# Kernel tuning notes

Hardware: AMD Instinct MI355X
Metric: run time of the kernel (lower is better)

## Reference

```python
import jax, jax.numpy as jnp
import numpy as np

D_MODEL = 1024
N_HEADS = 16
HEAD_DIM = D_MODEL // N_HEADS


def setup_inputs() -> dict:
    key = jax.random.key(0)
    k_x, k_qkv, k_out = jax.random.split(key, 3)
    x = jax.random.normal(k_x, (4, 2048, D_MODEL), dtype=jnp.float32)
    # nn.Linear weights are (out_features, in_features); init std=0.02
    w_qkv = jax.random.normal(k_qkv, (3 * D_MODEL, D_MODEL), dtype=jnp.float32) * 0.02
    w_out = jax.random.normal(k_out, (D_MODEL, D_MODEL), dtype=jnp.float32) * 0.02
    return {"x": x, "w_qkv": w_qkv, "w_out": w_out}


def reference(x, w_qkv, w_out):
    B, T, C = x.shape
    H, Dh = N_HEADS, HEAD_DIM
    # qkv projection: x @ w_qkv.T -> (B, T, 3C)
    qkv = jnp.einsum('btc,oc->bto', x, w_qkv)
    q, k, v = jnp.split(qkv, 3, axis=-1)

    def split_heads(t):
        return t.reshape(B, T, H, Dh).transpose(0, 2, 1, 3)  # (B, H, T, Dh)

    q, k, v = split_heads(q), split_heads(k), split_heads(v)
    scale = jnp.sqrt(jnp.asarray(Dh, dtype=x.dtype))
    scores = jnp.einsum('bhqd,bhkd->bhqk', q, k) / scale  # (B, H, T, T)
    causal = jnp.tril(jnp.ones((T, T), dtype=bool))
    scores = jnp.where(causal[None, None], scores, jnp.asarray(-jnp.inf, dtype=scores.dtype))
    attn = jax.nn.softmax(scores, axis=-1)
    out = jnp.einsum('bhqk,bhkd->bhqd', attn, v)  # (B, H, T, Dh)
    out = out.transpose(0, 2, 1, 3).reshape(B, T, C)
    return jnp.einsum('btc,oc->bto', out, w_out)
```

## Files before the change

### kernel.cpp

```cpp
#include <hip/hip_runtime.h>

typedef __attribute__((ext_vector_type(8))) short bf16x8;
typedef __attribute__((ext_vector_type(4))) float f32x4;
typedef __attribute__((ext_vector_type(16))) float f32x16;
typedef __attribute__((ext_vector_type(4))) int i32x4;
using u16 = unsigned short;

constexpr int Bsz = 4, T = 2048, C = 1024, H = 16, Dh = 64;
constexpr int Mrows = Bsz * T;
constexpr int K_DIM = 1024;
constexpr float QSCALE = 0.18033688011112042f;

__device__ inline u16 f2bf(float f) {
    unsigned u = __builtin_bit_cast(unsigned, f);
    u += 0x7FFFu + ((u >> 16) & 1u);
    return (u16)(u >> 16);
}

__device__ inline void g2l16(const void* g, void* l) {
    __builtin_amdgcn_global_load_lds((const __attribute__((address_space(1))) void*)g,
                                     (__attribute__((address_space(3))) void*)l, 16, 0, 0);
}

__device__ inline unsigned pk2(float lo, float hi) {
    unsigned d;
    asm("v_cvt_pk_bf16_f32 %0, %1, %2" : "=v"(d) : "v"(lo), "v"(hi));
    return d;
}
__device__ inline void swap32(unsigned& a, unsigned& b) {
    asm("v_permlane32_swap_b32 %0, %1" : "+v"(a), "+v"(b));
}

__global__ __launch_bounds__(256)
void cvt_k(const float* __restrict__ x, const float* __restrict__ wq,
           const float* __restrict__ wo, u16* __restrict__ xb,
           u16* __restrict__ wqb, u16* __restrict__ wob)
{
    int idx = blockIdx.x * 256 + threadIdx.x;
    const float* src; u16* dst; int rel;
    if (idx < 1048576)      { src = x;  dst = xb;  rel = idx; }
    else if (idx < 1441792) { src = wq; dst = wqb; rel = idx - 1048576; }
    else                    { src = wo; dst = wob; rel = idx - 1441792; }
    size_t off = (size_t)rel * 8;
    float4 a = *(const float4*)(src + off);
    float4 b = *(const float4*)(src + off + 4);
    unsigned r0 = (unsigned)f2bf(a.x) | ((unsigned)f2bf(a.y) << 16);
    unsigned r1 = (unsigned)f2bf(a.z) | ((unsigned)f2bf(a.w) << 16);
    unsigned r2 = (unsigned)f2bf(b.x) | ((unsigned)f2bf(b.y) << 16);
    unsigned r3 = (unsigned)f2bf(b.z) | ((unsigned)f2bf(b.w) << 16);
    *(uint4*)(dst + off) = make_uint4(r0, r1, r2, r3);
}

__device__ __forceinline__ bf16x8 rdfrag(const u16* base, int row, int kc, int lhi) {
    int byte = row * 128 + kc * 64 + lhi * 16;
    byte ^= (row & 7) << 4;
    return *(const bf16x8*)((const char*)base + byte);
}

__device__ __forceinline__ void stg_half(u16* ldsbase, const u16* gb, int tid) {
    #pragma unroll
    for (int it2 = 0; it2 < 2; ++it2) {
        int i = it2 * 512 + tid;
        int r = i >> 3, c8 = i & 7;
        int sc = c8 ^ (r & 7);
        g2l16(gb + (size_t)r * K_DIM + sc * 8,
              ldsbase + (size_t)(it2 * 512 + (tid & 448)) * 8);
    }
}

__device__ __forceinline__ void rdAf(bf16x8 (&af)[4][2], const u16* base,
                                     int r0, int lane16, int lhi) {
    #pragma unroll
    for (int mi = 0; mi < 4; ++mi)
        #pragma unroll
        for (int kc = 0; kc < 2; ++kc)
            af[mi][kc] = rdfrag(base, r0 + mi * 16 + lane16, kc, lhi);
}

__device__ __forceinline__ void rdBf(bf16x8 (&bf2)[2][2], const u16* base,
                                     int r0, int lane16, int lhi) {
    #pragma unroll
    for (int ni = 0; ni < 2; ++ni)
        #pragma unroll
        for (int kc = 0; kc < 2; ++kc)
            bf2[ni][kc] = rdfrag(base, r0 + ni * 16 + lane16, kc, lhi);
}

__device__ __forceinline__ void mfma_quad(f32x4 (&acc)[8][4], const bf16x8 (&af)[4][2],
                                          const bf16x8 (&bf2)[2][2], int rh, int ch) {
    #pragma unroll
    for (int kc = 0; kc < 2; ++kc)
        #pragma unroll
        for (int mi = 0; mi < 4; ++mi)
            #pragma unroll
            for (int ni = 0; ni < 2; ++ni)
                acc[rh * 4 + mi][ch * 2 + ni] = __builtin_amdgcn_mfma_f32_16x16x32_bf16(
                    af[mi][kc], bf2[ni][kc], acc[rh * 4 + mi][ch * 2 + ni], 0, 0, 0);
}

__device__ __forceinline__ void ph_open() {
    __builtin_amdgcn_s_barrier();
    asm volatile("s_waitcnt lgkmcnt(0)" ::: "memory");
    __builtin_amdgcn_sched_barrier(0);
}
__device__ __forceinline__ void ph_close() {
    __builtin_amdgcn_s_barrier();
    __builtin_amdgcn_sched_barrier(0);
}

__global__ __launch_bounds__(512, 2)
void gemm_qk8(const u16* __restrict__ xb, const u16* __restrict__ wqkvb,
              u16* __restrict__ qws, u16* __restrict__ kws)
{
    __shared__ alignas(16) u16 As[2][256 * 64];
    __shared__ alignas(16) u16 Bs2[2][256 * 64];

    const int tid = threadIdx.x;
    const int l = tid & 63, wid = tid >> 6;
    const int wm = wid >> 2, wn = wid & 3;
    const int lane16 = l & 15, lhi = l >> 4;
    const int m0 = blockIdx.x * 256, n0 = blockIdx.y * 256;

    const u16* Ab = xb + (size_t)m0 * K_DIM;
    const u16* Bb = wqkvb + (size_t)n0 * K_DIM;

    f32x4 acc[8][4] = {};
    bf16x8 af[4][2];
    bf16x8 bfr[2][2][2];

    stg_half(&As[0][0],     Ab, tid);
    stg_half(&As[0][8192],  Ab + (size_t)128 * K_DIM, tid);
    stg_half(&Bs2[0][0],    Bb, tid);
    stg_half(&Bs2[0][8192], Bb + (size_t)128 * K_DIM, tid);
    stg_half(&Bs2[1][0],    Bb + 64, tid);
    asm volatile("s_waitcnt vmcnt(2)" ::: "memory");
    __builtin_amdgcn_s_barrier();
    __builtin_amdgcn_sched_barrier(0);

    for (int it = 0; it < 8; ++it) {
        const int ka = it * 128;
        const bool more = (it < 7);

        rdAf(af, As[0], wm * 128, lane16, lhi);
        rdBf(bfr[0], Bs2[0], wn * 64, lane16, lhi);
        stg_half(&Bs2[1][8192], Bb + (size_t)128 * K_DIM + ka + 64, tid);
        ph_open();
        __builtin_amdgcn_s_setprio(1);
        mfma_quad(acc, af, bfr[0], 0, 0);
        __builtin_amdgcn_s_setprio(0);
        ph_close();

        rdBf(bfr[1], Bs2[0], wn * 64 + 32, lane16, lhi);
        stg_half(&As[1][0], Ab + ka + 64, tid);
        ph_open();
        __builtin_amdgcn_s_setprio(1);
        mfma_quad(acc, af, bfr[1], 0, 1);
        __builtin_amdgcn_s_setprio(0);
        ph_close();

        rdAf(af, As[0], wm * 128 + 64, lane16, lhi);
        stg_half(&As[1][8192], Ab + (size_t)128 * K_DIM + ka + 64, tid);
        ph_open();
        __builtin_amdgcn_s_setprio(1);
        mfma_quad(acc, af, bfr[1], 1, 1);
        __builtin_amdgcn_s_setprio(0);
        ph_close();

        if (more) stg_half(&Bs2[0][0], Bb + ka + 128, tid);
        ph_open();
        __builtin_amdgcn_s_setprio(1);
        mfma_quad(acc, af, bfr[0], 1, 0);
        __builtin_amdgcn_s_setprio(0);
        if (more) asm volatile("s_waitcnt vmcnt(2)" ::: "memory");
        else      asm volatile("s_waitcnt vmcnt(0)" ::: "memory");
        ph_close();

        rdAf(af, As[1], wm * 128, lane16, lhi);
        rdBf(bfr[0], Bs2[1], wn * 64, lane16, lhi);
        if (more) stg_half(&Bs2[0][8192], Bb + (size_t)128 * K_DIM + ka + 128, tid);
        ph_open();
        __builtin_amdgcn_s_setprio(1);
        mfma_quad(acc, af, bfr[0], 0, 0);
        __builtin_amdgcn_s_setprio(0);
        ph_close();

        rdBf(bfr[1], Bs2[1], wn * 64 + 32, lane16, lhi);
        if (more) stg_half(&As[0][0], Ab + ka + 128, tid);
        ph_open();
        __builtin_amdgcn_s_setprio(1);
        mfma_quad(acc, af, bfr[1], 0, 1);
        __builtin_amdgcn_s_setprio(0);
        ph_close();

        rdAf(af, As[1], wm * 128 + 64, lane16, lhi);
        if (more) stg_half(&As[0][8192], Ab + (size_t)128 * K_DIM + ka + 128, tid);
        ph_open();
        __builtin_amdgcn_s_setprio(1);
        mfma_quad(acc, af, bfr[1], 1, 1);
        __builtin_amdgcn_s_setprio(0);
        ph_close();

        if (more) stg_half(&Bs2[1][0], Bb + ka + 192, tid);
        ph_open();
        __builtin_amdgcn_s_setprio(1);
        mfma_quad(acc, af, bfr[0], 1, 0);
        __builtin_amdgcn_s_setprio(0);
        if (more) asm volatile("s_waitcnt vmcnt(2)" ::: "memory");
        else      asm volatile("s_waitcnt vmcnt(0)" ::: "memory");
        ph_close();
    }

    #pragma unroll
    for (int a = 0; a < 8; ++a)
        #pragma unroll
        for (int bc = 0; bc < 4; ++bc)
            #pragma unroll
            for (int r = 0; r < 4; ++r) {
                int gm = m0 + wm * 128 + a * 16 + lhi * 4 + r;
                int gn = n0 + wn * 64 + bc * 16 + lane16;
                float val = acc[a][bc][r];
                int hh = (gn >> 6) & 15, d = gn & 63;
                int bb = gm >> 11, t = gm & 2047;
                size_t off = (((size_t)bb * H + hh) * T + t) * Dh + d;
                if (gn < C) qws[off] = f2bf(val * QSCALE);
                else        kws[off] = f2bf(val);
            }
}

__device__ inline void stage_g(u16* lds, const u16* gb, int ldg, int tid) {
    #pragma unroll
    for (int i = 0; i < 4; ++i) {
        int ch = i * 256 + tid;
        int r = ch >> 3, c8 = ch & 7;
        int sc = c8 ^ (r & 7);
        g2l16(gb + (size_t)r * ldg + sc * 8, lds + (i * 256 + (tid & 192)) * 8);
    }
}

template<int MODE>
__device__ __forceinline__
void gemm_body(const u16* __restrict__ Ab, const u16* __restrict__ Bb,
               float* __restrict__ Op, u16* __restrict__ vtws,
               u16* As, u16* Bs, int m0, int n0)
{
    const int tid = threadIdx.x;
    const int l = tid & 63, wid = tid >> 6;
    const int wm = wid >> 1, wn = wid & 1;
    const int lane16 = l & 15, lhi = l >> 4;

    const u16* Abase = Ab + (size_t)m0 * K_DIM;
    const u16* Bbase = Bb + (size_t)n0 * K_DIM;

    f32x4 acc[4][4] = {};

    for (int ks = 0; ks < K_DIM / 64; ++ks) {
        __syncthreads();
        stage_g(As, Abase + ks * 64, K_DIM, tid);
        stage_g(Bs, Bbase + ks * 64, K_DIM, tid);
        __syncthreads();
        #pragma unroll
        for (int kc = 0; kc < 2; kc++) {
            bf16x8 af[4], bfr[4];
            #pragma unroll
            for (int mi = 0; mi < 4; mi++) {
                int row = wm * 64 + mi * 16 + lane16;
                int byte = row * 128 + kc * 64 + lhi * 16; byte ^= (row & 7) << 4;
                af[mi] = *(const bf16x8*)((const char*)As + byte);
            }
            #pragma unroll
            for (int ni = 0; ni < 4; ni++) {
                int row = wn * 64 + ni * 16 + lane16;
                int byte = row * 128 + kc * 64 + lhi * 16; byte ^= (row & 7) << 4;
                bfr[ni] = *(const bf16x8*)((const char*)Bs + byte);
            }
            #pragma unroll
            for (int mi = 0; mi < 4; mi++)
                #pragma unroll
                for (int ni = 0; ni < 4; ni++) {
                    if constexpr (MODE == 2)
                        acc[mi][ni] = __builtin_amdgcn_mfma_f32_16x16x32_bf16(
                            bfr[ni], af[mi], acc[mi][ni], 0, 0, 0);
                    else
                        acc[mi][ni] = __builtin_amdgcn_mfma_f32_16x16x32_bf16(
                            af[mi], bfr[ni], acc[mi][ni], 0, 0, 0);
                }
        }
    }

    if constexpr (MODE == 2) {
        #pragma unroll
        for (int mi = 0; mi < 4; mi++)
            #pragma unroll
            for (int ni = 0; ni < 4; ni++)
                #pragma unroll
                for (int r = 0; r < 4; r++) {
                    int wr = n0 + wn * 64 + ni * 16 + lhi * 4 + r;
                    int tg = m0 + wm * 64 + mi * 16 + lane16;
                    int hh = (wr >> 6) & 15, d = wr & 63;
                    int bb = tg >> 11, tt = tg & 2047;
                    size_t off = (((size_t)bb * H + hh) * Dh + d) * T + tt;
                    vtws[off] = f2bf(acc[mi][ni][r]);
                }
    } else {
        #pragma unroll
        for (int mi = 0; mi < 4; mi++)
            #pragma unroll
            for (int ni = 0; ni < 4; ni++)
                #pragma unroll
                for (int r = 0; r < 4; r++) {
                    int gm = m0 + wm * 64 + mi * 16 + lhi * 4 + r;
                    int gn = n0 + wn * 64 + ni * 16 + lane16;
                    Op[(size_t)gm * C + gn] = acc[mi][ni][r];
                }
    }
}

__global__ __launch_bounds__(256)
void gemm_v(const u16* __restrict__ xb, const u16* __restrict__ wqkvb,
            u16* __restrict__ vtws)
{
    __shared__ alignas(16) u16 As[128 * 64];
    __shared__ alignas(16) u16 Bs[128 * 64];
    gemm_body<2>(xb, wqkvb, nullptr, vtws, As, Bs,
                 blockIdx.x * 128, 2 * C + blockIdx.y * 128);
}

__global__ __launch_bounds__(256)
void gemm_out(const u16* __restrict__ ob, const u16* __restrict__ woutb,
              float* __restrict__ Op)
{
    __shared__ alignas(16) u16 As[128 * 64];
    __shared__ alignas(16) u16 Bs[128 * 64];
    gemm_body<1>(ob, woutb, Op, nullptr, As, Bs,
                 blockIdx.x * 128, blockIdx.y * 128);
}

constexpr float SMAX = 16.0f;

__device__ inline void stage_c(u16* lds, const u16* gb, int rstride, int tid) {
    #pragma unroll
    for (int it = 0; it < 2; ++it) {
        int i = it * 256 + tid;
        int r = i & 63, c8 = i >> 6;
        g2l16(gb + (size_t)r * rstride + c8 * 8, lds + i * 8);
    }
}

__global__ __launch_bounds__(256, 3)
void attn_k(const u16* __restrict__ qws, const u16* __restrict__ kws,
            const u16* __restrict__ vtws, u16* __restrict__ ows)
{
    __shared__ alignas(16) u16 KL[3][64 * 64];
    __shared__ alignas(16) u16 VL[3][64 * 64];

    const int bid = blockIdx.x;
    const int head = bid & 63;
    const int qt = 15 - (bid >> 6);
    const int b = head >> 4, h = head & 15;
    const int tid = threadIdx.x, w = tid >> 6, l = tid & 63;
    const int l31 = l & 31, hi = l >> 5;

    const size_t hoff = (size_t)head * (T * Dh);
    const u16* Qg  = qws + hoff;
    const u16* Kg  = kws + hoff;
    const u16* Vtg = vtws + hoff;

    const int qb = qt * 128;
    const int nt = 2 * qt + 2;
    const int qbw = qb + w * 32;

    bf16x8 qf[4];
    #pragma unroll
    for (int c = 0; c < 4; ++c)
        qf[c] = *(const bf16x8*)(Qg + (size_t)(qbw + l31) * Dh + c * 16 + hi * 8);

    f32x16 o0{}, o1{};
    float lrun = 0.f;

    stage_c(KL[0], Kg, Dh, tid);
    stage_c(VL[0], Vtg, T, tid);
    stage_c(KL[1], Kg + (size_t)64 * Dh, Dh, tid);
    stage_c(VL[1], Vtg + 64, T, tid);

    int cur = 0;
    for (int t = 0; t < nt; ++t) {
        if (t + 1 < nt) asm volatile("s_waitcnt vmcnt(4)" ::: "memory");
        else            asm volatile("s_waitcnt vmcnt(0)" ::: "memory");
        __builtin_amdgcn_s_barrier();
        __builtin_amdgcn_sched_barrier(0);

        int nx = cur + 2; if (nx >= 3) nx -= 3;
        if (t + 2 < nt) {
            stage_c(KL[nx], Kg + (size_t)(t + 2) * 64 * Dh, Dh, tid);
            stage_c(VL[nx], Vtg + (t + 2) * 64, T, tid);
        }

        const int kv0 = t * 64;
        if (kv0 <= qbw + 31) {
            const char* Kb = (const char*)KL[cur];
            const char* Vb = (const char*)VL[cur];

            bf16x8 kf0[4], kf1[4];
            #pragma unroll
            for (int c = 0; c < 4; ++c) {
                int off = (c * 2 + hi) * 1024 + l31 * 16;
                kf0[c] = *(const bf16x8*)(Kb + off);
                kf1[c] = *(const bf16x8*)(Kb + off + 512);
            }

            f32x16 s0{}, s1{};
            __builtin_amdgcn_s_setprio(1);
            #pragma unroll
            for (int c = 0; c < 4; ++c) {
                s0 = __builtin_amdgcn_mfma_f32_32x32x16_bf16(kf0[c], qf[c], s0, 0, 0, 0);
                s1 = __builtin_amdgcn_mfma_f32_32x32x16_bf16(kf1[c], qf[c], s1, 0, 0, 0);
            }
            __builtin_amdgcn_s_setprio(0);

            if (kv0 + 63 > qbw) {
                int qg = qbw + l31;
                #pragma unroll
                for (int r = 0; r < 16; ++r) {
                    int kvg = kv0 + (r & 3) + 8 * (r >> 2) + 4 * hi;
                    if (kvg > qg)      s0[r] = -__builtin_inff();
                    if (kvg + 32 > qg) s1[r] = -__builtin_inff();
                }
            }

            float p0[16], p1[16];
            float t0 = 0.f, t1 = 0.f, t2 = 0.f, t3 = 0.f;
            #pragma unroll
            for (int r = 0; r < 16; ++r) {
                p0[r] = __builtin_amdgcn_exp2f(s0[r] - SMAX);
                p1[r] = __builtin_amdgcn_exp2f(s1[r] - SMAX);
                float s = p0[r] + p1[r];
                if ((r & 3) == 0) t0 += s; else if ((r & 3) == 1) t1 += s;
                else if ((r & 3) == 2) t2 += s; else t3 += s;
            }
            lrun += (t0 + t1) + (t2 + t3);

            unsigned paf[4][4];
            unsigned cc[8];
            #pragma unroll
            for (int i = 0; i < 4; ++i) cc[i]     = pk2(p0[2 * i], p0[2 * i + 1]);
            #pragma unroll
            for (int i = 0; i < 4; ++i) cc[4 + i] = pk2(p0[8 + 2 * i], p0[9 + 2 * i]);
            swap32(cc[0], cc[2]); swap32(cc[1], cc[3]);
            swap32(cc[4], cc[6]); swap32(cc[5], cc[7]);
            #pragma unroll
            for (int i = 0; i < 4; ++i) { paf[0][i] = cc[i]; paf[1][i] = cc[4 + i]; }
            #pragma unroll
            for (int i = 0; i < 4; ++i) cc[i]     = pk2(p1[2 * i], p1[2 * i + 1]);
            #pragma unroll
            for (int i = 0; i < 4; ++i) cc[4 + i] = pk2(p1[8 + 2 * i], p1[9 + 2 * i]);
            swap32(cc[0], cc[2]); swap32(cc[1], cc[3]);
            swap32(cc[4], cc[6]); swap32(cc[5], cc[7]);
            #pragma unroll
            for (int i = 0; i < 4; ++i) { paf[2][i] = cc[i]; paf[3][i] = cc[4 + i]; }

            __builtin_amdgcn_s_setprio(1);
            #pragma unroll
            for (int kb = 0; kb < 4; ++kb) {
                i32x4 wv = {(int)paf[kb][0], (int)paf[kb][1],
                            (int)paf[kb][2], (int)paf[kb][3]};
                bf16x8 pa = __builtin_bit_cast(bf16x8, wv);
                int off = (kb * 2 + hi) * 1024 + l31 * 16;
                bf16x8 v0 = *(const bf16x8*)(Vb + off);
                bf16x8 v1 = *(const bf16x8*)(Vb + off + 512);
                o0 = __builtin_amdgcn_mfma_f32_32x32x16_bf16(pa, v0, o0, 0, 0, 0);
                o1 = __builtin_amdgcn_mfma_f32_32x32x16_bf16(pa, v1, o1, 0, 0, 0);
            }
            __builtin_amdgcn_s_setprio(0);
        }
        cur = (cur == 2) ? 0 : cur + 1;
    }

    float lt = lrun + __shfl_xor(lrun, 32);
    float inv = 1.0f / lt;
    #pragma unroll
    for (int r = 0; r < 16; ++r) {
        int cr = (r & 3) + 8 * (r >> 2) + 4 * hi;
        float il = __shfl(inv, cr);
        size_t rowoff = ((size_t)b * T + qb + w * 32 + cr) * C + h * Dh + l31;
        ows[rowoff]      = f2bf(o0[r] * il);
        ows[rowoff + 32] = f2bf(o1[r] * il);
    }
}

extern "C" void kernel_launch(void* const* d_in, const int* in_sizes, int n_in,
                              void* d_out, int out_size, void* d_ws, size_t ws_size,
                              hipStream_t stream)
{
    const float* x     = (const float*)d_in[0];
    const float* w_qkv = (const float*)d_in[1];
    const float* w_out = (const float*)d_in[2];
    float* out = (float*)d_out;

    const size_t SZ = (size_t)Bsz * H * T * Dh;
    u16* qws   = (u16*)d_ws;
    u16* kws   = qws + SZ;
    u16* vtws  = kws + SZ;
    u16* xb    = vtws + SZ;
    u16* ows   = xb;
    u16* wqkvb = xb + SZ;
    u16* woutb = wqkvb + (size_t)3 * C * C;

    cvt_k<<<dim3(6144), 256, 0, stream>>>(x, w_qkv, w_out, xb, wqkvb, woutb);

    gemm_qk8<<<dim3(Mrows / 256, (2 * C) / 256), 512, 0, stream>>>(xb, wqkvb, qws, kws);
    gemm_v<<<dim3(Mrows / 128, C / 128), 256, 0, stream>>>(xb, wqkvb, vtws);

    attn_k<<<dim3(1024), 256, 0, stream>>>(qws, kws, vtws, ows);

    gemm_out<<<dim3(Mrows / 128, C / 128), 256, 0, stream>>>(ows, woutb, out);
}
```

Before: 154.9 us.

## Software-pipeline attention loop: QK^T of tile t overlapped with softmax/PV of t-1

Restructures the causal attention inner loop so each iteration issues the QK^T MFMAs for the current KV tile while the exp, packing and PV MFMAs run for the previous tile's saved scores. V tiles are now staged one tile ahead instead of two, and a final drain step finishes the last tile after the loop. The goal is to hide softmax VALU/transcendental latency behind matrix-core work. It costs extra live registers for the carried score accumulators and drops the setprio hints.

```diff
diff --git a/kernel.cpp b/kernel.cpp
--- a/kernel.cpp
+++ b/kernel.cpp
@@ -376,30 +376,73 @@
 
     f32x16 o0{}, o1{};
     float lrun = 0.f;
+    f32x16 sp0{}, sp1{};
+
+    auto fin = [&](int slot) {
+        const char* Vb = (const char*)VL[slot];
+        float p0[16], p1[16];
+        float t0 = 0.f, t1 = 0.f, t2 = 0.f, t3 = 0.f;
+        #pragma unroll
+        for (int r = 0; r < 16; ++r) {
+            p0[r] = __builtin_amdgcn_exp2f(sp0[r] - SMAX);
+            p1[r] = __builtin_amdgcn_exp2f(sp1[r] - SMAX);
+            float s = p0[r] + p1[r];
+            if ((r & 3) == 0) t0 += s; else if ((r & 3) == 1) t1 += s;
+            else if ((r & 3) == 2) t2 += s; else t3 += s;
+        }
+        lrun += (t0 + t1) + (t2 + t3);
+
+        unsigned paf[4][4];
+        unsigned cc[8];
+        #pragma unroll
+        for (int i = 0; i < 4; ++i) cc[i]     = pk2(p0[2 * i], p0[2 * i + 1]);
+        #pragma unroll
+        for (int i = 0; i < 4; ++i) cc[4 + i] = pk2(p0[8 + 2 * i], p0[9 + 2 * i]);
+        swap32(cc[0], cc[2]); swap32(cc[1], cc[3]);
+        swap32(cc[4], cc[6]); swap32(cc[5], cc[7]);
+        #pragma unroll
+        for (int i = 0; i < 4; ++i) { paf[0][i] = cc[i]; paf[1][i] = cc[4 + i]; }
+        #pragma unroll
+        for (int i = 0; i < 4; ++i) cc[i]     = pk2(p1[2 * i], p1[2 * i + 1]);
+        #pragma unroll
+        for (int i = 0; i < 4; ++i) cc[4 + i] = pk2(p1[8 + 2 * i], p1[9 + 2 * i]);
+        swap32(cc[0], cc[2]); swap32(cc[1], cc[3]);
+        swap32(cc[4], cc[6]); swap32(cc[5], cc[7]);
+        #pragma unroll
+        for (int i = 0; i < 4; ++i) { paf[2][i] = cc[i]; paf[3][i] = cc[4 + i]; }
+
+        #pragma unroll
+        for (int kb = 0; kb < 4; ++kb) {
+            i32x4 wv = {(int)paf[kb][0], (int)paf[kb][1],
+                        (int)paf[kb][2], (int)paf[kb][3]};
+            bf16x8 pa = __builtin_bit_cast(bf16x8, wv);
+            int off = (kb * 2 + hi) * 1024 + l31 * 16;
+            bf16x8 v0 = *(const bf16x8*)(Vb + off);
+            bf16x8 v1 = *(const bf16x8*)(Vb + off + 512);
+            o0 = __builtin_amdgcn_mfma_f32_32x32x16_bf16(pa, v0, o0, 0, 0, 0);
+            o1 = __builtin_amdgcn_mfma_f32_32x32x16_bf16(pa, v1, o1, 0, 0, 0);
+        }
+    };
 
     stage_c(KL[0], Kg, Dh, tid);
+    stage_c(KL[1], Kg + (size_t)64 * Dh, Dh, tid);
     stage_c(VL[0], Vtg, T, tid);
-    stage_c(KL[1], Kg + (size_t)64 * Dh, Dh, tid);
-    stage_c(VL[1], Vtg + 64, T, tid);
-
-    int cur = 0;
+
     for (int t = 0; t < nt; ++t) {
         if (t + 1 < nt) asm volatile("s_waitcnt vmcnt(4)" ::: "memory");
         else            asm volatile("s_waitcnt vmcnt(0)" ::: "memory");
         __builtin_amdgcn_s_barrier();
         __builtin_amdgcn_sched_barrier(0);
 
-        int nx = cur + 2; if (nx >= 3) nx -= 3;
-        if (t + 2 < nt) {
-            stage_c(KL[nx], Kg + (size_t)(t + 2) * 64 * Dh, Dh, tid);
-            stage_c(VL[nx], Vtg + (t + 2) * 64, T, tid);
-        }
+        int tp2 = t + 2; while (tp2 >= 3) tp2 -= 3;
+        int tp1 = t + 1; while (tp1 >= 3) tp1 -= 3;
+        int tm1 = t + 2; while (tm1 >= 3) tm1 -= 3;
+        if (t + 2 < nt) stage_c(KL[tp2], Kg + (size_t)(t + 2) * 64 * Dh, Dh, tid);
+        if (t + 1 < nt) stage_c(VL[tp1], Vtg + (t + 1) * 64, T, tid);
 
         const int kv0 = t * 64;
         if (kv0 <= qbw + 31) {
-            const char* Kb = (const char*)KL[cur];
-            const char* Vb = (const char*)VL[cur];
-
+            const char* Kb = (const char*)KL[t % 3];
             bf16x8 kf0[4], kf1[4];
             #pragma unroll
             for (int c = 0; c < 4; ++c) {
@@ -427,52 +470,15 @@
                 }
             }
 
-            float p0[16], p1[16];
-            float t0 = 0.f, t1 = 0.f, t2 = 0.f, t3 = 0.f;
-            #pragma unroll
-            for (int r = 0; r < 16; ++r) {
-                p0[r] = __builtin_amdgcn_exp2f(s0[r] - SMAX);
-                p1[r] = __builtin_amdgcn_exp2f(s1[r] - SMAX);
-                float s = p0[r] + p1[r];
-                if ((r & 3) == 0) t0 += s; else if ((r & 3) == 1) t1 += s;
-                else if ((r & 3) == 2) t2 += s; else t3 += s;
-            }
-            lrun += (t0 + t1) + (t2 + t3);
-
-            unsigned paf[4][4];
-            unsigned cc[8];
-            #pragma unroll
-            for (int i = 0; i < 4; ++i) cc[i]     = pk2(p0[2 * i], p0[2 * i + 1]);
-            #pragma unroll
-            for (int i = 0; i < 4; ++i) cc[4 + i] = pk2(p0[8 + 2 * i], p0[9 + 2 * i]);
-            swap32(cc[0], cc[2]); swap32(cc[1], cc[3]);
-            swap32(cc[4], cc[6]); swap32(cc[5], cc[7]);
-            #pragma unroll
-            for (int i = 0; i < 4; ++i) { paf[0][i] = cc[i]; paf[1][i] = cc[4 + i]; }
-            #pragma unroll
-            for (int i = 0; i < 4; ++i) cc[i]     = pk2(p1[2 * i], p1[2 * i + 1]);
-            #pragma unroll
-            for (int i = 0; i < 4; ++i) cc[4 + i] = pk2(p1[8 + 2 * i], p1[9 + 2 * i]);
-            swap32(cc[0], cc[2]); swap32(cc[1], cc[3]);
-            swap32(cc[4], cc[6]); swap32(cc[5], cc[7]);
-            #pragma unroll
-            for (int i = 0; i < 4; ++i) { paf[2][i] = cc[i]; paf[3][i] = cc[4 + i]; }
-
-            __builtin_amdgcn_s_setprio(1);
-            #pragma unroll
-            for (int kb = 0; kb < 4; ++kb) {
-                i32x4 wv = {(int)paf[kb][0], (int)paf[kb][1],
-                            (int)paf[kb][2], (int)paf[kb][3]};
-                bf16x8 pa = __builtin_bit_cast(bf16x8, wv);
-                int off = (kb * 2 + hi) * 1024 + l31 * 16;
-                bf16x8 v0 = *(const bf16x8*)(Vb + off);
-                bf16x8 v1 = *(const bf16x8*)(Vb + off + 512);
-                o0 = __builtin_amdgcn_mfma_f32_32x32x16_bf16(pa, v0, o0, 0, 0, 0);
-                o1 = __builtin_amdgcn_mfma_f32_32x32x16_bf16(pa, v1, o1, 0, 0, 0);
-            }
-            __builtin_amdgcn_s_setprio(0);
+            if (t > 0) fin(tm1);
+            sp0 = s0; sp1 = s1;
+        } else if (kv0 <= qbw + 95) {
+            fin(tm1);
         }
-        cur = (cur == 2) ? 0 : cur + 1;
+    }
+    if ((nt - 1) * 64 <= qbw + 31) {
+        int slot = nt - 1; while (slot >= 3) slot -= 3;
+        fin(slot);
     }
 
     float lt = lrun + __shfl_xor(lrun, 32);
```

New measurement: 155.3 us. About the same (+0.2%).

## Double attention query tile per block to reuse staged K/V across two query subtiles

Applied to the files above, without the earlier changes.

Each attention block now handles 256 query rows (64 per wave, two 32-row subtiles) instead of 128. The grid halves to 512 blocks. Every K/V tile staged into LDS and every K/V fragment loaded into registers now feeds two query subtiles, which halves global-to-LDS K/V traffic and LDS fragment reads per unit of work. In exchange, register pressure rises (launch bounds drop from 3 to 2 blocks per CU), the grid is smaller, and causal load imbalance across blocks grows.

```diff
diff --git a/kernel.cpp b/kernel.cpp
--- a/kernel.cpp
+++ b/kernel.cpp
@@ -346,7 +346,7 @@
     }
 }
 
-__global__ __launch_bounds__(256, 3)
+__global__ __launch_bounds__(256, 2)
 void attn_k(const u16* __restrict__ qws, const u16* __restrict__ kws,
             const u16* __restrict__ vtws, u16* __restrict__ ows)
 {
@@ -355,7 +355,7 @@
 
     const int bid = blockIdx.x;
     const int head = bid & 63;
-    const int qt = 15 - (bid >> 6);
+    const int qt = 7 - (bid >> 6);
     const int b = head >> 4, h = head & 15;
     const int tid = threadIdx.x, w = tid >> 6, l = tid & 63;
     const int l31 = l & 31, hi = l >> 5;
@@ -365,17 +365,20 @@
     const u16* Kg  = kws + hoff;
     const u16* Vtg = vtws + hoff;
 
-    const int qb = qt * 128;
-    const int nt = 2 * qt + 2;
-    const int qbw = qb + w * 32;
-
-    bf16x8 qf[4];
-    #pragma unroll
-    for (int c = 0; c < 4; ++c)
-        qf[c] = *(const bf16x8*)(Qg + (size_t)(qbw + l31) * Dh + c * 16 + hi * 8);
-
-    f32x16 o0{}, o1{};
-    float lrun = 0.f;
+    const int qb = qt * 256;
+    const int nt = 4 * qt + 4;
+    const int qbw = qb + w * 64;
+
+    bf16x8 qf[2][4];
+    #pragma unroll
+    for (int q2 = 0; q2 < 2; ++q2)
+        #pragma unroll
+        for (int c = 0; c < 4; ++c)
+            qf[q2][c] = *(const bf16x8*)(Qg + (size_t)(qbw + q2 * 32 + l31) * Dh
+                                         + c * 16 + hi * 8);
+
+    f32x16 oq[2][2] = {};
+    float lrun[2] = {0.f, 0.f};
 
     stage_c(KL[0], Kg, Dh, tid);
     stage_c(VL[0], Vtg, T, tid);
@@ -396,94 +399,102 @@
         }
 
         const int kv0 = t * 64;
-        if (kv0 <= qbw + 31) {
+        if (kv0 <= qbw + 63) {
             const char* Kb = (const char*)KL[cur];
             const char* Vb = (const char*)VL[cur];
 
-            bf16x8 kf0[4], kf1[4];
+            bf16x8 kf0[4], kf1[4], vf0[4], vf1[4];
             #pragma unroll
             for (int c = 0; c < 4; ++c) {
                 int off = (c * 2 + hi) * 1024 + l31 * 16;
                 kf0[c] = *(const bf16x8*)(Kb + off);
                 kf1[c] = *(const bf16x8*)(Kb + off + 512);
+                vf0[c] = *(const bf16x8*)(Vb + off);
+                vf1[c] = *(const bf16x8*)(Vb + off + 512);
             }
 
-            f32x16 s0{}, s1{};
-            __builtin_amdgcn_s_setprio(1);
-            #pragma unroll
-            for (int c = 0; c < 4; ++c) {
-                s0 = __builtin_amdgcn_mfma_f32_32x32x16_bf16(kf0[c], qf[c], s0, 0, 0, 0);
-                s1 = __builtin_amdgcn_mfma_f32_32x32x16_bf16(kf1[c], qf[c], s1, 0, 0, 0);
+            #pragma unroll
+            for (int q2 = 0; q2 < 2; ++q2) {
+                const int qbb = qbw + q2 * 32;
+                if (kv0 > qbb + 31) continue;
+
+                f32x16 s0{}, s1{};
+                __builtin_amdgcn_s_setprio(1);
+                #pragma unroll
+                for (int c = 0; c < 4; ++c) {
+                    s0 = __builtin_amdgcn_mfma_f32_32x32x16_bf16(kf0[c], qf[q2][c], s0, 0, 0, 0);
+                    s1 = __builtin_amdgcn_mfma_f32_32x32x16_bf16(kf1[c], qf[q2][c], s1, 0, 0, 0);
+                }
+                __builtin_amdgcn_s_setprio(0);
+
+                if (kv0 + 63 > qbb) {
+                    int qg = qbb + l31;
+                    #pragma unroll
+                    for (int r = 0; r < 16; ++r) {
+                        int kvg = kv0 + (r & 3) + 8 * (r >> 2) + 4 * hi;
+                        if (kvg > qg)      s0[r] = -__builtin_inff();
+                        if (kvg + 32 > qg) s1[r] = -__builtin_inff();
+                    }
+                }
+
+                float p0[16], p1[16];
+                float t0 = 0.f, t1 = 0.f, t2 = 0.f, t3 = 0.f;
+                #pragma unroll
+                for (int r = 0; r < 16; ++r) {
+                    p0[r] = __builtin_amdgcn_exp2f(s0[r] - SMAX);
+                    p1[r] = __builtin_amdgcn_exp2f(s1[r] - SMAX);
+                    float s = p0[r] + p1[r];
+                    if ((r & 3) == 0) t0 += s; else if ((r & 3) == 1) t1 += s;
+                    else if ((r & 3) == 2) t2 += s; else t3 += s;
+                }
+                lrun[q2] += (t0 + t1) + (t2 + t3);
+
+                unsigned paf[4][4];
+                unsigned cc[8];
+                #pragma unroll
+                for (int i = 0; i < 4; ++i) cc[i]     = pk2(p0[2 * i], p0[2 * i + 1]);
+                #pragma unroll
+                for (int i = 0; i < 4; ++i) cc[4 + i] = pk2(p0[8 + 2 * i], p0[9 + 2 * i]);
+                swap32(cc[0], cc[2]); swap32(cc[1], cc[3]);
+                swap32(cc[4], cc[6]); swap32(cc[5], cc[7]);
+                #pragma unroll
+                for (int i = 0; i < 4; ++i) { paf[0][i] = cc[i]; paf[1][i] = cc[4 + i]; }
+                #pragma unroll
+                for (int i = 0; i < 4; ++i) cc[i]     = pk2(p1[2 * i], p1[2 * i + 1]);
+                #pragma unroll
+                for (int i = 0; i < 4; ++i) cc[4 + i] = pk2(p1[8 + 2 * i], p1[9 + 2 * i]);
+                swap32(cc[0], cc[2]); swap32(cc[1], cc[3]);
+                swap32(cc[4], cc[6]); swap32(cc[5], cc[7]);
+                #pragma unroll
+                for (int i = 0; i < 4; ++i) { paf[2][i] = cc[i]; paf[3][i] = cc[4 + i]; }
+
+                __builtin_amdgcn_s_setprio(1);
+                #pragma unroll
+                for (int kb = 0; kb < 4; ++kb) {
+                    i32x4 wv = {(int)paf[kb][0], (int)paf[kb][1],
+                                (int)paf[kb][2], (int)paf[kb][3]};
+                    bf16x8 pa = __builtin_bit_cast(bf16x8, wv);
+                    oq[q2][0] = __builtin_amdgcn_mfma_f32_32x32x16_bf16(pa, vf0[kb], oq[q2][0], 0, 0, 0);
+                    oq[q2][1] = __builtin_amdgcn_mfma_f32_32x32x16_bf16(pa, vf1[kb], oq[q2][1], 0, 0, 0);
+                }
+                __builtin_amdgcn_s_setprio(0);
             }
-            __builtin_amdgcn_s_setprio(0);
-
-            if (kv0 + 63 > qbw) {
-                int qg = qbw + l31;
-                #pragma unroll
-                for (int r = 0; r < 16; ++r) {
-                    int kvg = kv0 + (r & 3) + 8 * (r >> 2) + 4 * hi;
-                    if (kvg > qg)      s0[r] = -__builtin_inff();
-                    if (kvg + 32 > qg) s1[r] = -__builtin_inff();
-                }
-            }
-
-            float p0[16], p1[16];
-            float t0 = 0.f, t1 = 0.f, t2 = 0.f, t3 = 0.f;
-            #pragma unroll
-            for (int r = 0; r < 16; ++r) {
-                p0[r] = __builtin_amdgcn_exp2f(s0[r] - SMAX);
-                p1[r] = __builtin_amdgcn_exp2f(s1[r] - SMAX);
-                float s = p0[r] + p1[r];
-                if ((r & 3) == 0) t0 += s; else if ((r & 3) == 1) t1 += s;
-                else if ((r & 3) == 2) t2 += s; else t3 += s;
-            }
-            lrun += (t0 + t1) + (t2 + t3);
-
-            unsigned paf[4][4];
-            unsigned cc[8];
-            #pragma unroll
-            for (int i = 0; i < 4; ++i) cc[i]     = pk2(p0[2 * i], p0[2 * i + 1]);
-            #pragma unroll
-            for (int i = 0; i < 4; ++i) cc[4 + i] = pk2(p0[8 + 2 * i], p0[9 + 2 * i]);
-            swap32(cc[0], cc[2]); swap32(cc[1], cc[3]);
-            swap32(cc[4], cc[6]); swap32(cc[5], cc[7]);
-            #pragma unroll
-            for (int i = 0; i < 4; ++i) { paf[0][i] = cc[i]; paf[1][i] = cc[4 + i]; }
-            #pragma unroll
-            for (int i = 0; i < 4; ++i) cc[i]     = pk2(p1[2 * i], p1[2 * i + 1]);
-            #pragma unroll
-            for (int i = 0; i < 4; ++i) cc[4 + i] = pk2(p1[8 + 2 * i], p1[9 + 2 * i]);
-            swap32(cc[0], cc[2]); swap32(cc[1], cc[3]);
-            swap32(cc[4], cc[6]); swap32(cc[5], cc[7]);
-            #pragma unroll
-            for (int i = 0; i < 4; ++i) { paf[2][i] = cc[i]; paf[3][i] = cc[4 + i]; }
-
-            __builtin_amdgcn_s_setprio(1);
-            #pragma unroll
-            for (int kb = 0; kb < 4; ++kb) {
-                i32x4 wv = {(int)paf[kb][0], (int)paf[kb][1],
-                            (int)paf[kb][2], (int)paf[kb][3]};
-                bf16x8 pa = __builtin_bit_cast(bf16x8, wv);
-                int off = (kb * 2 + hi) * 1024 + l31 * 16;
-                bf16x8 v0 = *(const bf16x8*)(Vb + off);
-                bf16x8 v1 = *(const bf16x8*)(Vb + off + 512);
-                o0 = __builtin_amdgcn_mfma_f32_32x32x16_bf16(pa, v0, o0, 0, 0, 0);
-                o1 = __builtin_amdgcn_mfma_f32_32x32x16_bf16(pa, v1, o1, 0, 0, 0);
-            }
-            __builtin_amdgcn_s_setprio(0);
         }
         cur = (cur == 2) ? 0 : cur + 1;
     }
 
-    float lt = lrun + __shfl_xor(lrun, 32);
-    float inv = 1.0f / lt;
-    #pragma unroll
-    for (int r = 0; r < 16; ++r) {
-        int cr = (r & 3) + 8 * (r >> 2) + 4 * hi;
-        float il = __shfl(inv, cr);
-        size_t rowoff = ((size_t)b * T + qb + w * 32 + cr) * C + h * Dh + l31;
-        ows[rowoff]      = f2bf(o0[r] * il);
-        ows[rowoff + 32] = f2bf(o1[r] * il);
+    #pragma unroll
+    for (int q2 = 0; q2 < 2; ++q2) {
+        float lt = lrun[q2] + __shfl_xor(lrun[q2], 32);
+        float inv = 1.0f / lt;
+        #pragma unroll
+        for (int r = 0; r < 16; ++r) {
+            int cr = (r & 3) + 8 * (r >> 2) + 4 * hi;
+            float il = __shfl(inv, cr);
+            size_t rowoff = ((size_t)b * T + qbw + q2 * 32 + cr) * C + h * Dh + l31;
+            ows[rowoff]      = f2bf(oq[q2][0][r] * il);
+            ows[rowoff + 32] = f2bf(oq[q2][1][r] * il);
+        }
     }
 }
 
@@ -510,7 +521,7 @@
     gemm_qk8<<<dim3(Mrows / 256, (2 * C) / 256), 512, 0, stream>>>(xb, wqkvb, qws, kws);
     gemm_v<<<dim3(Mrows / 128, C / 128), 256, 0, stream>>>(xb, wqkvb, vtws);
 
-    attn_k<<<dim3(1024), 256, 0, stream>>>(qws, kws, vtws, ows);
+    attn_k<<<dim3(512), 256, 0, stream>>>(qws, kws, vtws, ows);
 
     gemm_out<<<dim3(Mrows / 128, C / 128), 256, 0, stream>>>(ows, woutb, out);
 }
```

New measurement: 166.2 us. 1.07x slower.
